# Performance work log

Hardware: AMD Instinct MI355X
Metric: run time of the kernel (lower is better)

The kernel has to match this reference:

```python
import jax, jax.numpy as jnp
import numpy as np

N_POINTS = 200000
B, H, W, K = 16, 299, 299, 8


def setup_inputs() -> dict:
    key = jax.random.key(0)
    k1, k2, k3, k4 = jax.random.split(key, 4)
    spatial_rgb = jax.random.normal(k1, (N_POINTS, 4), dtype=jnp.float32)
    weights = jax.random.uniform(k2, (B, H, W, K), dtype=jnp.float32)
    idx = jax.random.randint(k3, (B, H, W, K), 0, N_POINTS).astype(jnp.float32)
    weight_and_index_list = jnp.stack([weights, idx], axis=1)  # (B,2,H,W,K)
    ori_img = jax.random.uniform(k4, (B, H, W, 4), dtype=jnp.float32) * 255.0
    return {"spatial_rgb": spatial_rgb,
            "weight_and_index_list": weight_and_index_list,
            "ori_img": ori_img}


def reference(spatial_rgb, weight_and_index_list, ori_img):
    # s: flat (N,4) RGBA table
    s = spatial_rgb.reshape(-1, 4)
    w = weight_and_index_list[:, 0]                      # (B,H,W,K) weights
    idx = weight_and_index_list[:, 1].astype(jnp.int32)  # (B,H,W,K) flat indices

    # gather (B,H,W,K,4), weighted sum over K -> (B,H,W,4)
    gathered = s[idx]
    x = jnp.sum(gathered * w[..., None], axis=-2)

    alpha = x[..., 3:4] / 255.0          # (B,H,W,1)
    ori_alpha = ori_img[..., 3:4]

    # epsilon is None -> unclipped branch
    x_rgb = ori_img[..., :3] + x[..., :3] * alpha
    x_rgb = jnp.where(ori_alpha > 0, x_rgb, jnp.zeros_like(x_rgb))
    x_rgba = jnp.clip(jnp.concatenate([x_rgb, ori_alpha], axis=-1), 0.0, 255.0)

    # NHWC -> NCHW (transpose(2,3).transpose(1,2))
    cla_x = jnp.transpose(x_rgba, (0, 3, 1, 2))
    cla_ori = jnp.transpose(ori_img, (0, 3, 1, 2))

    def alpha_to_white(img_nchw):
        a = img_nchw[:, 3:4]
        return jnp.where(a > 0, img_nchw[:, :3], jnp.full_like(img_nchw[:, :3], 255.0))

    # model_name == 'my_model': no resize; classifier stubbed as identity
    cla = alpha_to_white(cla_x)
    ori_cla = alpha_to_white(cla_ori)
    return (x, x_rgba, cla, ori_img, ori_cla)
```

## Files before the change

kernel.cpp:

```cpp
#include <hip/hip_runtime.h>

#define BB 16
#define HH 299
#define WW 299
#define KK 8
#define HWPIX (HH * WW)
#define NPIX (BB * HWPIX)
#define PPT 2
#define TPB 256
#define SPAN (TPB * PPT)

typedef float f4 __attribute__((ext_vector_type(4)));

__global__ __launch_bounds__(TPB, 4) void gauss_net_kernel(
    const f4* __restrict__ spatial,
    const f4* __restrict__ wi4,
    const f4* __restrict__ ori,
    float* __restrict__ out)
{
    const int tbase = blockIdx.x * SPAN + threadIdx.x;

    f4*    out_x    = (f4*)out;
    f4*    out_rgba = out_x + NPIX;
    float* out_cla  = (float*)(out_rgba + NPIX);
    f4*    out_ori  = (f4*)(out_cla + (size_t)BB * 3 * HWPIX);
    float* out_ocla = (float*)(out_ori + NPIX);

    int  p[PPT], bidx[PPT], rem[PPT];
    bool act[PPT];
    f4   w0[PPT], w1[PPT], i0[PPT], i1[PPT], o[PPT];

#pragma unroll
    for (int u = 0; u < PPT; ++u) {
        p[u]   = tbase + u * TPB;
        act[u] = (p[u] < NPIX);
        int pc = act[u] ? p[u] : 0;
        bidx[u] = pc / HWPIX;
        rem[u]  = pc - bidx[u] * HWPIX;
        size_t wb = ((size_t)(2 * bidx[u]) * HWPIX + rem[u]) * 2;
        size_t ib = wb + (size_t)HWPIX * 2;
        w0[u] = __builtin_nontemporal_load(wi4 + wb);
        w1[u] = __builtin_nontemporal_load(wi4 + wb + 1);
        i0[u] = __builtin_nontemporal_load(wi4 + ib);
        i1[u] = __builtin_nontemporal_load(wi4 + ib + 1);
        o[u]  = __builtin_nontemporal_load(ori + pc);
    }

    f4 g[PPT][KK];
#pragma unroll
    for (int u = 0; u < PPT; ++u) {
        int id[KK] = { (int)i0[u].x, (int)i0[u].y, (int)i0[u].z, (int)i0[u].w,
                       (int)i1[u].x, (int)i1[u].y, (int)i1[u].z, (int)i1[u].w };
#pragma unroll
        for (int k = 0; k < KK; ++k) g[u][k] = spatial[id[k]];
    }

#pragma unroll
    for (int u = 0; u < PPT; ++u) {
        if (!act[u]) continue;
        float wt[KK] = { w0[u].x, w0[u].y, w0[u].z, w0[u].w,
                         w1[u].x, w1[u].y, w1[u].z, w1[u].w };
        f4 acc = (f4){0.f, 0.f, 0.f, 0.f};
#pragma unroll
        for (int k = 0; k < KK; ++k) acc += g[u][k] * wt[k];

        f4 ov = o[u];
        float alpha = acc.w * (1.0f / 255.0f);
        float r  = fmaf(acc.x, alpha, ov.x);
        float gr = fmaf(acc.y, alpha, ov.y);
        float bl = fmaf(acc.z, alpha, ov.z);
        bool oa_pos = (ov.w > 0.0f);
        if (!oa_pos) { r = 0.f; gr = 0.f; bl = 0.f; }

        float cr = fminf(fmaxf(r,  0.f), 255.f);
        float cg = fminf(fmaxf(gr, 0.f), 255.f);
        float cb = fminf(fmaxf(bl, 0.f), 255.f);
        float ca = fminf(fmaxf(ov.w, 0.f), 255.f);

        __builtin_nontemporal_store(acc, out_x + p[u]);
        __builtin_nontemporal_store((f4){cr, cg, cb, ca}, out_rgba + p[u]);
        __builtin_nontemporal_store(ov, out_ori + p[u]);

        size_t cbase = (size_t)bidx[u] * 3 * HWPIX + rem[u];
        bool ca_pos = (ca > 0.0f);
        __builtin_nontemporal_store(ca_pos ? cr : 255.0f, out_cla + cbase);
        __builtin_nontemporal_store(ca_pos ? cg : 255.0f, out_cla + cbase + HWPIX);
        __builtin_nontemporal_store(ca_pos ? cb : 255.0f, out_cla + cbase + 2 * HWPIX);

        __builtin_nontemporal_store(oa_pos ? ov.x : 255.0f, out_ocla + cbase);
        __builtin_nontemporal_store(oa_pos ? ov.y : 255.0f, out_ocla + cbase + HWPIX);
        __builtin_nontemporal_store(oa_pos ? ov.z : 255.0f, out_ocla + cbase + 2 * HWPIX);
    }
}

extern "C" void kernel_launch(void* const* d_in, const int* in_sizes, int n_in,
                              void* d_out, int out_size, void* d_ws, size_t ws_size,
                              hipStream_t stream) {
    const f4* spatial = (const f4*)d_in[0];
    const f4* wi4     = (const f4*)d_in[1];
    const f4* ori     = (const f4*)d_in[2];
    float* out = (float*)d_out;

    int blocks = (NPIX + SPAN - 1) / SPAN;
    gauss_net_kernel<<<blocks, TPB, 0, stream>>>(spatial, wi4, ori, out);
}
```

Before: 232.9 us.

## Process four consecutive pixels per thread to vectorize planar NCHW stores

After: 370.1 us. 58.9% more time.

```diff
diff --git a/kernel.cpp b/kernel.cpp
--- a/kernel.cpp
+++ b/kernel.cpp
@@ -6,11 +6,13 @@
 #define KK 8
 #define HWPIX (HH * WW)
 #define NPIX (BB * HWPIX)
-#define PPT 2
+#define GPB (HWPIX / 4)
+#define NGROUPS (BB * GPB)
+#define NTHREADS (NGROUPS + BB)
 #define TPB 256
-#define SPAN (TPB * PPT)
 
 typedef float f4 __attribute__((ext_vector_type(4)));
+typedef f4 uf4 __attribute__((aligned(4)));
 
 __global__ __launch_bounds__(TPB, 4) void gauss_net_kernel(
     const f4* __restrict__ spatial,
@@ -18,7 +20,8 @@
     const f4* __restrict__ ori,
     float* __restrict__ out)
 {
-    const int tbase = blockIdx.x * SPAN + threadIdx.x;
+    const int gid = blockIdx.x * TPB + threadIdx.x;
+    if (gid >= NTHREADS) return;
 
     f4*    out_x    = (f4*)out;
     f4*    out_rgba = out_x + NPIX;
@@ -26,45 +29,106 @@
     f4*    out_ori  = (f4*)(out_cla + (size_t)BB * 3 * HWPIX);
     float* out_ocla = (float*)(out_ori + NPIX);
 
-    int  p[PPT], bidx[PPT], rem[PPT];
-    bool act[PPT];
-    f4   w0[PPT], w1[PPT], i0[PPT], i1[PPT], o[PPT];
+    if (gid < NGROUPS) {
+        const int b   = gid / GPB;
+        const int rem = (gid - b * GPB) * 4;
+        const size_t p  = (size_t)b * HWPIX + rem;
+        const size_t wb = ((size_t)(2 * b) * HWPIX + rem) * 2;
+        const size_t ib = wb + (size_t)2 * HWPIX;
 
+        f4 w[4][2], iv[4][2], o[4];
 #pragma unroll
-    for (int u = 0; u < PPT; ++u) {
-        p[u]   = tbase + u * TPB;
-        act[u] = (p[u] < NPIX);
-        int pc = act[u] ? p[u] : 0;
-        bidx[u] = pc / HWPIX;
-        rem[u]  = pc - bidx[u] * HWPIX;
-        size_t wb = ((size_t)(2 * bidx[u]) * HWPIX + rem[u]) * 2;
-        size_t ib = wb + (size_t)HWPIX * 2;
-        w0[u] = __builtin_nontemporal_load(wi4 + wb);
-        w1[u] = __builtin_nontemporal_load(wi4 + wb + 1);
-        i0[u] = __builtin_nontemporal_load(wi4 + ib);
-        i1[u] = __builtin_nontemporal_load(wi4 + ib + 1);
-        o[u]  = __builtin_nontemporal_load(ori + pc);
-    }
+        for (int j = 0; j < 4; ++j) {
+            w[j][0]  = __builtin_nontemporal_load(wi4 + wb + 2 * j);
+            w[j][1]  = __builtin_nontemporal_load(wi4 + wb + 2 * j + 1);
+            iv[j][0] = __builtin_nontemporal_load(wi4 + ib + 2 * j);
+            iv[j][1] = __builtin_nontemporal_load(wi4 + ib + 2 * j + 1);
+            o[j]     = __builtin_nontemporal_load(ori + p + j);
+        }
 
-    f4 g[PPT][KK];
+        f4 g[4][KK];
 #pragma unroll
-    for (int u = 0; u < PPT; ++u) {
-        int id[KK] = { (int)i0[u].x, (int)i0[u].y, (int)i0[u].z, (int)i0[u].w,
-                       (int)i1[u].x, (int)i1[u].y, (int)i1[u].z, (int)i1[u].w };
+        for (int j = 0; j < 4; ++j) {
+            int id[KK] = { (int)iv[j][0].x, (int)iv[j][0].y, (int)iv[j][0].z, (int)iv[j][0].w,
+                           (int)iv[j][1].x, (int)iv[j][1].y, (int)iv[j][1].z, (int)iv[j][1].w };
 #pragma unroll
-        for (int k = 0; k < KK; ++k) g[u][k] = spatial[id[k]];
-    }
+            for (int k = 0; k < KK; ++k) g[j][k] = spatial[id[k]];
+        }
 
+        float cr[4], cg[4], cb[4], ca[4];
+        float or_[4], og_[4], ob_[4];
+        bool  oa[4];
 #pragma unroll
-    for (int u = 0; u < PPT; ++u) {
-        if (!act[u]) continue;
-        float wt[KK] = { w0[u].x, w0[u].y, w0[u].z, w0[u].w,
-                         w1[u].x, w1[u].y, w1[u].z, w1[u].w };
+        for (int j = 0; j < 4; ++j) {
+            float wt[KK] = { w[j][0].x, w[j][0].y, w[j][0].z, w[j][0].w,
+                             w[j][1].x, w[j][1].y, w[j][1].z, w[j][1].w };
+            f4 acc = (f4){0.f, 0.f, 0.f, 0.f};
+#pragma unroll
+            for (int k = 0; k < KK; ++k) acc += g[j][k] * wt[k];
+
+            f4 ov = o[j];
+            float alpha = acc.w * (1.0f / 255.0f);
+            float r  = fmaf(acc.x, alpha, ov.x);
+            float gr = fmaf(acc.y, alpha, ov.y);
+            float bl = fmaf(acc.z, alpha, ov.z);
+            oa[j] = (ov.w > 0.0f);
+            if (!oa[j]) { r = 0.f; gr = 0.f; bl = 0.f; }
+
+            cr[j] = fminf(fmaxf(r,  0.f), 255.f);
+            cg[j] = fminf(fmaxf(gr, 0.f), 255.f);
+            cb[j] = fminf(fmaxf(bl, 0.f), 255.f);
+            ca[j] = fminf(fmaxf(ov.w, 0.f), 255.f);
+            or_[j] = ov.x; og_[j] = ov.y; ob_[j] = ov.z;
+
+            __builtin_nontemporal_store(acc, out_x + p + j);
+            __builtin_nontemporal_store((f4){cr[j], cg[j], cb[j], ca[j]}, out_rgba + p + j);
+            __builtin_nontemporal_store(ov, out_ori + p + j);
+        }
+
+        const size_t cbase = (size_t)b * 3 * HWPIX + rem;
+        f4 vcr = { oa[0] ? cr[0] : 255.f, oa[1] ? cr[1] : 255.f,
+                   oa[2] ? cr[2] : 255.f, oa[3] ? cr[3] : 255.f };
+        f4 vcg = { oa[0] ? cg[0] : 255.f, oa[1] ? cg[1] : 255.f,
+                   oa[2] ? cg[2] : 255.f, oa[3] ? cg[3] : 255.f };
+        f4 vcb = { oa[0] ? cb[0] : 255.f, oa[1] ? cb[1] : 255.f,
+                   oa[2] ? cb[2] : 255.f, oa[3] ? cb[3] : 255.f };
+        __builtin_nontemporal_store(vcr, (uf4*)(out_cla + cbase));
+        __builtin_nontemporal_store(vcg, (uf4*)(out_cla + cbase + HWPIX));
+        __builtin_nontemporal_store(vcb, (uf4*)(out_cla + cbase + 2 * (size_t)HWPIX));
+
+        f4 vor = { oa[0] ? or_[0] : 255.f, oa[1] ? or_[1] : 255.f,
+                   oa[2] ? or_[2] : 255.f, oa[3] ? or_[3] : 255.f };
+        f4 vog = { oa[0] ? og_[0] : 255.f, oa[1] ? og_[1] : 255.f,
+                   oa[2] ? og_[2] : 255.f, oa[3] ? og_[3] : 255.f };
+        f4 vob = { oa[0] ? ob_[0] : 255.f, oa[1] ? ob_[1] : 255.f,
+                   oa[2] ? ob_[2] : 255.f, oa[3] ? ob_[3] : 255.f };
+        __builtin_nontemporal_store(vor, (uf4*)(out_ocla + cbase));
+        __builtin_nontemporal_store(vog, (uf4*)(out_ocla + cbase + HWPIX));
+        __builtin_nontemporal_store(vob, (uf4*)(out_ocla + cbase + 2 * (size_t)HWPIX));
+    } else {
+        const int b   = gid - NGROUPS;
+        const int rem = HWPIX - 1;
+        const size_t p  = (size_t)b * HWPIX + rem;
+        const size_t wb = ((size_t)(2 * b) * HWPIX + rem) * 2;
+        const size_t ib = wb + (size_t)2 * HWPIX;
+
+        f4 w0 = __builtin_nontemporal_load(wi4 + wb);
+        f4 w1 = __builtin_nontemporal_load(wi4 + wb + 1);
+        f4 i0 = __builtin_nontemporal_load(wi4 + ib);
+        f4 i1 = __builtin_nontemporal_load(wi4 + ib + 1);
+        f4 ov = __builtin_nontemporal_load(ori + p);
+
+        int id[KK] = { (int)i0.x, (int)i0.y, (int)i0.z, (int)i0.w,
+                       (int)i1.x, (int)i1.y, (int)i1.z, (int)i1.w };
+        f4 g[KK];
+#pragma unroll
+        for (int k = 0; k < KK; ++k) g[k] = spatial[id[k]];
+
+        float wt[KK] = { w0.x, w0.y, w0.z, w0.w, w1.x, w1.y, w1.z, w1.w };
         f4 acc = (f4){0.f, 0.f, 0.f, 0.f};
 #pragma unroll
-        for (int k = 0; k < KK; ++k) acc += g[u][k] * wt[k];
+        for (int k = 0; k < KK; ++k) acc += g[k] * wt[k];
 
-        f4 ov = o[u];
         float alpha = acc.w * (1.0f / 255.0f);
         float r  = fmaf(acc.x, alpha, ov.x);
         float gr = fmaf(acc.y, alpha, ov.y);
@@ -77,19 +141,19 @@
         float cb = fminf(fmaxf(bl, 0.f), 255.f);
         float ca = fminf(fmaxf(ov.w, 0.f), 255.f);
 
-        __builtin_nontemporal_store(acc, out_x + p[u]);
-        __builtin_nontemporal_store((f4){cr, cg, cb, ca}, out_rgba + p[u]);
-        __builtin_nontemporal_store(ov, out_ori + p[u]);
+        __builtin_nontemporal_store(acc, out_x + p);
+        __builtin_nontemporal_store((f4){cr, cg, cb, ca}, out_rgba + p);
+        __builtin_nontemporal_store(ov, out_ori + p);
 
-        size_t cbase = (size_t)bidx[u] * 3 * HWPIX + rem[u];
+        const size_t cbase = (size_t)b * 3 * HWPIX + rem;
         bool ca_pos = (ca > 0.0f);
         __builtin_nontemporal_store(ca_pos ? cr : 255.0f, out_cla + cbase);
         __builtin_nontemporal_store(ca_pos ? cg : 255.0f, out_cla + cbase + HWPIX);
-        __builtin_nontemporal_store(ca_pos ? cb : 255.0f, out_cla + cbase + 2 * HWPIX);
+        __builtin_nontemporal_store(ca_pos ? cb : 255.0f, out_cla + cbase + 2 * (size_t)HWPIX);
 
         __builtin_nontemporal_store(oa_pos ? ov.x : 255.0f, out_ocla + cbase);
         __builtin_nontemporal_store(oa_pos ? ov.y : 255.0f, out_ocla + cbase + HWPIX);
-        __builtin_nontemporal_store(oa_pos ? ov.z : 255.0f, out_ocla + cbase + 2 * HWPIX);
+        __builtin_nontemporal_store(oa_pos ? ov.z : 255.0f, out_ocla + cbase + 2 * (size_t)HWPIX);
     }
 }
 
@@ -101,6 +165,6 @@
     const f4* ori     = (const f4*)d_in[2];
     float* out = (float*)d_out;
 
-    int blocks = (NPIX + SPAN - 1) / SPAN;
+    int blocks = (NTHREADS + TPB - 1) / TPB;
     gauss_net_kernel<<<blocks, TPB, 0, stream>>>(spatial, wi4, ori, out);
 }
```
